# Kernel optimization log

Measured on AMD Instinct MI355X. Metric: run time of the kernel, lower is better.

## Reference

```python
import jax, jax.numpy as jnp
import numpy as np

S, HID = 2048, 4096
H, KV, D = 32, 8, 128
EPS = 1e-6
THETA = 10000.0


def setup_inputs() -> dict:
    key = jax.random.key(0)
    k0, k1, k2 = jax.random.split(key, 3)
    return {
        "positions": jnp.arange(S, dtype=jnp.int32),
        "hidden_states": jax.random.normal(k0, (S, HID), jnp.float32),
        "w_qkv": jax.random.normal(k1, ((H + 2 * KV) * D, HID), jnp.float32) * 0.02,
        "w_o": jax.random.normal(k2, (HID, H * D), jnp.float32) * 0.02,
        "gq": jnp.ones((D,), jnp.float32),
        "gk": jnp.ones((D,), jnp.float32),
    }


def _rmsnorm(x, g):
    # per-head RMSNorm over last dim (head_dim)
    return x * jax.lax.rsqrt(jnp.mean(x * x, axis=-1, keepdims=True) + EPS) * g


def _rope(x, positions):
    # NeoX-style rotary embedding, rotary_dim == head_dim
    half = D // 2
    inv_freq = 1.0 / (THETA ** (jnp.arange(half, dtype=jnp.float32) * 2.0 / D))
    freqs = positions.astype(jnp.float32)[:, None] * inv_freq  # [S, half]
    cos = jnp.cos(freqs)[:, None, :]  # [S, 1, half]
    sin = jnp.sin(freqs)[:, None, :]
    x1, x2 = x[..., :half], x[..., half:]
    return jnp.concatenate([x1 * cos - x2 * sin, x2 * cos + x1 * sin], axis=-1)


def reference(positions, hidden_states, w_qkv, w_o, gq, gk):
    qkv = hidden_states @ w_qkv.T  # [S, (H+2KV)*D]
    q = qkv[:, : H * D].reshape(S, H, D)
    k = qkv[:, H * D : (H + KV) * D].reshape(S, KV, D)
    v = qkv[:, (H + KV) * D :].reshape(S, KV, D)

    q = _rmsnorm(q, gq)
    k = _rmsnorm(k, gk)
    q = _rope(q, positions)
    k = _rope(k, positions)

    rep = H // KV
    kf = jnp.repeat(k, rep, axis=1)  # [S, H, D]
    vf = jnp.repeat(v, rep, axis=1)

    scale = D ** -0.5
    scores = jnp.einsum("qhd,khd->hqk", q, kf) * scale  # [H, S, S]
    causal = jnp.tril(jnp.ones((S, S), dtype=bool))
    scores = jnp.where(causal[None], scores, jnp.finfo(scores.dtype).min)
    attn = jax.nn.softmax(scores, axis=-1)
    ctx = jnp.einsum("hqk,khd->qhd", attn, vf).reshape(S, H * D)
    return ctx @ w_o.T  # [S, HID]
```

## Files before the change

kernel.cpp:

```cpp
#include <hip/hip_runtime.h>
#include <hip/hip_bf16.h>

#define S_LEN 2048
#define HID   4096
#define NH    32
#define NKV   8
#define DH    128
#define NQKV  ((NH + 2*NKV) * DH)

typedef __attribute__((ext_vector_type(8))) short s16x8;
typedef __attribute__((ext_vector_type(4))) short s16x4;
typedef __attribute__((ext_vector_type(4))) float f32x4;

__device__ __forceinline__ short f2bf(float x) {
    union { __hip_bfloat16 b; short s; } u;
    u.b = __float2bfloat16(x);
    return u.s;
}
__device__ __forceinline__ float bf2f(short s) {
    union { unsigned int u; float f; } v;
    v.u = ((unsigned int)(unsigned short)s) << 16;
    return v.f;
}

__device__ __forceinline__ void gload16(const void* g, void* l) {
    __builtin_amdgcn_global_load_lds(
        (const __attribute__((address_space(1))) void*)g,
        (__attribute__((address_space(3))) void*)l,
        16, 0, 0);
}

__device__ __forceinline__ void cstore(float* p, float v) { *p = v; }
__device__ __forceinline__ void cstore(short* p, float v) { *p = f2bf(v); }

__global__ __launch_bounds__(256) void convert_hs_wqkv(
        const float* __restrict__ in1, short* __restrict__ o1, long n1,
        const float* __restrict__ in2, short* __restrict__ o2, long n2)
{
    const long total = n1 + n2;
    long i0 = ((long)blockIdx.x * blockDim.x + threadIdx.x) * 4;
    long stride = (long)gridDim.x * blockDim.x * 4;
    for (long i = i0; i < total; i += stride) {
        const float* src; short* dst; long off;
        if (i < n1) { src = in1; dst = o1; off = i; }
        else        { src = in2; dst = o2; off = i - n1; }
        float4 v = *(const float4*)(src + off);
        s16x4 o;
        o[0] = f2bf(v.x); o[1] = f2bf(v.y); o[2] = f2bf(v.z); o[3] = f2bf(v.w);
        *(s16x4*)(dst + off) = o;
    }
}

template <typename OT>
__global__ __launch_bounds__(256, 2) void gemm192(
        const short* __restrict__ A, const short* __restrict__ B,
        OT* __restrict__ C, int M, int N, int K)
{
    __shared__ char lds[81920];
    const int t = threadIdx.x;
    const int w = t >> 6, l = t & 63, g = l >> 4, q16 = l & 15;
    const int wm = w >> 1, wn = w & 1;
    const int bx = blockIdx.x, by = blockIdx.y;
    const int NT = K >> 6;

    const int srow = t >> 3;
    const int schunk = (t & 7) ^ (srow & 7);
    unsigned goffA[4], goffB[6];
#pragma unroll
    for (int i = 0; i < 4; ++i)
        goffA[i] = (unsigned)(((by * 128 + i * 32 + srow) * K) * 2 + schunk * 16);
#pragma unroll
    for (int i = 0; i < 6; ++i)
        goffB[i] = (unsigned)(((bx * 192 + i * 32 + srow) * K) * 2 + schunk * 16);
    const int dstw = w * 1024;

    auto STAGE = [&](int kt) {
        const int par = kt & 1;
        char* dA = lds + par * 16384 + dstw;
        char* dB = lds + 32768 + par * 24576 + dstw;
        const unsigned kb = (unsigned)kt * 128;
#pragma unroll
        for (int i = 0; i < 4; ++i)
            gload16((const char*)A + (goffA[i] + kb), dA + i * 4096);
#pragma unroll
        for (int i = 0; i < 6; ++i)
            gload16((const char*)B + (goffB[i] + kb), dB + i * 4096);
    };

    int aoff[4], boff[6];
#pragma unroll
    for (int mi = 0; mi < 4; ++mi) aoff[mi] = (wm * 64 + mi * 16 + q16) * 128;
#pragma unroll
    for (int ni = 0; ni < 6; ++ni) boff[ni] = (wn * 96 + ni * 16 + q16) * 128;
    const int sw0 = ((g) ^ (q16 & 7)) << 4;
    const int sw1 = ((4 + g) ^ (q16 & 7)) << 4;

    f32x4 acc[4][6] = {};
    s16x8 aE[4][2], aO[4][2], b0f[3][2], b1f[3][2];

    STAGE(0); STAGE(1);
    asm volatile("s_waitcnt vmcnt(10)" ::: "memory");
    __builtin_amdgcn_s_barrier();
    {
        const char* A0 = lds;
#pragma unroll
        for (int mi = 0; mi < 4; ++mi) {
            aE[mi][0] = *(const s16x8*)(A0 + aoff[mi] + sw0);
            aE[mi][1] = *(const s16x8*)(A0 + aoff[mi] + sw1);
        }
    }

#define GB(KT, AC, AN, PAR) do {                                              \
    const char* Bs_ = lds + 32768 + (PAR) * 24576;                            \
    _Pragma("unroll")                                                         \
    for (int ni = 0; ni < 3; ++ni) {                                          \
        b0f[ni][0] = *(const s16x8*)(Bs_ + boff[ni] + sw0);                   \
        b0f[ni][1] = *(const s16x8*)(Bs_ + boff[ni] + sw1);                   \
    }                                                                         \
    _Pragma("unroll")                                                         \
    for (int ni = 0; ni < 3; ++ni) {                                          \
        b1f[ni][0] = *(const s16x8*)(Bs_ + boff[3 + ni] + sw0);               \
        b1f[ni][1] = *(const s16x8*)(Bs_ + boff[3 + ni] + sw1);               \
    }                                                                         \
    asm volatile("s_waitcnt lgkmcnt(6)" ::: "memory");       \
    __builtin_amdgcn_sched_barrier(0);                                        \
    __builtin_amdgcn_s_setprio(1);                                            \
    _Pragma("unroll")                                                         \
    for (int mi = 0; mi < 4; ++mi)                                            \
    _Pragma("unroll")                                                         \
    for (int ni = 0; ni < 3; ++ni)                                            \
    _Pragma("unroll")                                                         \
    for (int kk = 0; kk < 2; ++kk)                                            \
        acc[mi][ni] = __builtin_amdgcn_mfma_f32_16x16x32_bf16(                \
                AC[mi][kk], b0f[ni][kk], acc[mi][ni], 0, 0, 0);               \
    __builtin_amdgcn_s_setprio(0);                                            \
    asm volatile("s_waitcnt lgkmcnt(0)" ::: "memory");           \
    __builtin_amdgcn_sched_barrier(0);                                        \
    asm volatile("s_waitcnt vmcnt(0)" ::: "memory");        \
    __builtin_amdgcn_s_barrier();       \
    if ((KT) + 2 < NT) STAGE((KT) + 2);                                       \
    if ((KT) + 1 < NT) {                      \
        const char* An_ = lds + (((PAR) ^ 1) * 16384);                        \
        _Pragma("unroll")                                                     \
        for (int mi = 0; mi < 4; ++mi) {                                      \
            AN[mi][0] = *(const s16x8*)(An_ + aoff[mi] + sw0);                \
            AN[mi][1] = *(const s16x8*)(An_ + aoff[mi] + sw1);                \
        }                                                                     \
    }                                                                         \
    __builtin_amdgcn_s_setprio(1);                                            \
    _Pragma("unroll")                                                         \
    for (int mi = 0; mi < 4; ++mi)                                            \
    _Pragma("unroll")                                                         \
    for (int ni = 0; ni < 3; ++ni)                                            \
    _Pragma("unroll")                                                         \
    for (int kk = 0; kk < 2; ++kk)                                            \
        acc[mi][3 + ni] = __builtin_amdgcn_mfma_f32_16x16x32_bf16(            \
                AC[mi][kk], b1f[ni][kk], acc[mi][3 + ni], 0, 0, 0);           \
    __builtin_amdgcn_s_setprio(0);                                            \
} while (0)

    for (int kt = 0; kt < NT; kt += 2) {
        GB(kt,     aE, aO, 0);
        GB(kt + 1, aO, aE, 1);
    }
#undef GB

#pragma unroll
    for (int mi = 0; mi < 4; ++mi) {
        long row = (long)by * 128 + wm * 64 + mi * 16 + g * 4;
#pragma unroll
        for (int ni = 0; ni < 6; ++ni) {
            long col = (long)bx * 192 + wn * 96 + ni * 16 + q16;
            f32x4 v = acc[mi][ni];
#pragma unroll
            for (int r = 0; r < 4; ++r)
                cstore(&C[(row + r) * (long)N + col], v[r]);
        }
    }
}

template <typename OT>
__global__ __launch_bounds__(256, 2) void gemm_bt(
        const short* __restrict__ A, const short* __restrict__ B,
        OT* __restrict__ C, int M, int N, int K)
{
    __shared__ char lds[65536];
    const int t = threadIdx.x;
    const int w = t >> 6, l = t & 63, g = l >> 4, q16 = l & 15;
    const int wm = w >> 1, wn = w & 1;
    const int bx = blockIdx.x, by = blockIdx.y;
    const int NT = K >> 6;

    const int srow = t >> 3;
    const int schunk = (t & 7) ^ (srow & 7);
    unsigned goffA[4], goffB[4];
#pragma unroll
    for (int i = 0; i < 4; ++i) {
        goffA[i] = (unsigned)(((by * 128 + i * 32 + srow) * K) * 2 + schunk * 16);
        goffB[i] = (unsigned)(((bx * 128 + i * 32 + srow) * K) * 2 + schunk * 16);
    }
    const int dstw = w * 1024;

    auto STAGE = [&](int kt) {
        const int par = kt & 1;
        char* dA = lds + par * 16384 + dstw;
        char* dB = lds + 32768 + par * 16384 + dstw;
        const unsigned kb = (unsigned)kt * 128;
#pragma unroll
        for (int i = 0; i < 4; ++i) {
            gload16((const char*)A + (goffA[i] + kb), dA + i * 4096);
            gload16((const char*)B + (goffB[i] + kb), dB + i * 4096);
        }
    };

    int aoff[4], boff[4];
#pragma unroll
    for (int i = 0; i < 4; ++i) {
        aoff[i] = (wm * 64 + i * 16 + q16) * 128;
        boff[i] = (wn * 64 + i * 16 + q16) * 128;
    }
    const int sw0 = ((g) ^ (q16 & 7)) << 4;
    const int sw1 = ((4 + g) ^ (q16 & 7)) << 4;

    f32x4 acc[4][4] = {};
    s16x8 aE[4][2], aO[4][2], bf[4][2];

    STAGE(0); STAGE(1);
    asm volatile("s_waitcnt vmcnt(8)" ::: "memory");
    __builtin_amdgcn_s_barrier();
    {
        const char* A0 = lds;
#pragma unroll
        for (int mi = 0; mi < 4; ++mi) {
            aE[mi][0] = *(const s16x8*)(A0 + aoff[mi] + sw0);
            aE[mi][1] = *(const s16x8*)(A0 + aoff[mi] + sw1);
        }
    }

#define GB(KT, AC, AN, PAR) do {                                              \
    const char* Bs_ = lds + 32768 + (PAR) * 16384;                            \
    _Pragma("unroll")                                                         \
    for (int ni = 0; ni < 4; ++ni) {                                          \
        bf[ni][0] = *(const s16x8*)(Bs_ + boff[ni] + sw0);                    \
        bf[ni][1] = *(const s16x8*)(Bs_ + boff[ni] + sw1);                    \
    }                                                                         \
    asm volatile("s_waitcnt lgkmcnt(4)" ::: "memory");      \
    __builtin_amdgcn_sched_barrier(0);                                        \
    __builtin_amdgcn_s_setprio(1);                                            \
    _Pragma("unroll")                                                         \
    for (int mi = 0; mi < 4; ++mi)                                            \
    _Pragma("unroll")                                                         \
    for (int ni = 0; ni < 2; ++ni)                                            \
    _Pragma("unroll")                                                         \
    for (int kk = 0; kk < 2; ++kk)                                            \
        acc[mi][ni] = __builtin_amdgcn_mfma_f32_16x16x32_bf16(                \
                AC[mi][kk], bf[ni][kk], acc[mi][ni], 0, 0, 0);                \
    __builtin_amdgcn_s_setprio(0);                                            \
    asm volatile("s_waitcnt lgkmcnt(0)" ::: "memory");          \
    __builtin_amdgcn_sched_barrier(0);                                        \
    asm volatile("s_waitcnt vmcnt(0)" ::: "memory");        \
    __builtin_amdgcn_s_barrier();       \
    if ((KT) + 2 < NT) STAGE((KT) + 2);                                       \
    if ((KT) + 1 < NT) {                      \
        const char* An_ = lds + (((PAR) ^ 1) * 16384);                        \
        _Pragma("unroll")                                                     \
        for (int mi = 0; mi < 4; ++mi) {                                      \
            AN[mi][0] = *(const s16x8*)(An_ + aoff[mi] + sw0);                \
            AN[mi][1] = *(const s16x8*)(An_ + aoff[mi] + sw1);                \
        }                                                                     \
    }                                                                         \
    __builtin_amdgcn_s_setprio(1);                                            \
    _Pragma("unroll")                                                         \
    for (int mi = 0; mi < 4; ++mi)                                            \
    _Pragma("unroll")                                                         \
    for (int ni = 0; ni < 2; ++ni)                                            \
    _Pragma("unroll")                                                         \
    for (int kk = 0; kk < 2; ++kk)                                            \
        acc[mi][2 + ni] = __builtin_amdgcn_mfma_f32_16x16x32_bf16(            \
                AC[mi][kk], bf[2 + ni][kk], acc[mi][2 + ni], 0, 0, 0);        \
    __builtin_amdgcn_s_setprio(0);                                            \
} while (0)

    for (int kt = 0; kt < NT; kt += 2) {
        GB(kt,     aE, aO, 0);
        GB(kt + 1, aO, aE, 1);
    }
#undef GB

#pragma unroll
    for (int mi = 0; mi < 4; ++mi) {
        long row = (long)by * 128 + wm * 64 + mi * 16 + g * 4;
#pragma unroll
        for (int ni = 0; ni < 4; ++ni) {
            long col = (long)bx * 128 + wn * 64 + ni * 16 + q16;
            f32x4 v = acc[mi][ni];
#pragma unroll
            for (int r = 0; r < 4; ++r)
                cstore(&C[(row + r) * (long)N + col], v[r]);
        }
    }
}

__global__ __launch_bounds__(256) void post_gemm1_fused(
        const float* __restrict__ wo, short* __restrict__ wob,
        const short* __restrict__ qkvb, const int* __restrict__ pos,
        const float* __restrict__ gq, const float* __restrict__ gk,
        short* __restrict__ qo, short* __restrict__ ko,
        short* __restrict__ vt)
{
    const int bid = blockIdx.x;

    if (bid < 2048) {
        const long n = (long)HID * (NH * DH);
        long i0 = ((long)bid * 256 + threadIdx.x) * 4;
        long stride = 2048L * 256 * 4;
        for (long i = i0; i < n; i += stride) {
            float4 v = *(const float4*)(wo + i);
            s16x4 o;
            o[0] = f2bf(v.x); o[1] = f2bf(v.y); o[2] = f2bf(v.z); o[3] = f2bf(v.w);
            *(s16x4*)(wob + i) = o;
        }
        return;
    }

    if (bid < 12288) {
        const int idx = bid - 2048;
        const int s = idx / 5;
        const int slot = (idx % 5) * 8 + (threadIdx.x >> 5);
        const int p = threadIdx.x & 31, d = p * 4;

        s16x4 xv = *(const s16x4*)(qkvb + (long)s * NQKV + slot * DH + d);
        float x[4];
#pragma unroll
        for (int r = 0; r < 4; ++r) x[r] = bf2f(xv[r]);

        float ss = x[0]*x[0] + x[1]*x[1] + x[2]*x[2] + x[3]*x[3];
#pragma unroll
        for (int o = 1; o < 32; o <<= 1) ss += __shfl_xor(ss, o);
        float rms = rsqrtf(ss * (1.0f / DH) + 1e-6f);

        const bool isq = slot < NH;
        const float* gp = isq ? gq : gk;
        float y[4];
#pragma unroll
        for (int r = 0; r < 4; ++r) y[r] = x[r] * rms * gp[d + r];

        float y2[4];
#pragma unroll
        for (int r = 0; r < 4; ++r) y2[r] = __shfl_xor(y[r], 16);

        const float po = (float)pos[s];
        const int jbase = d & 63;
        s16x4 ov;
#pragma unroll
        for (int r = 0; r < 4; ++r) {
            float invf = exp2f(-(float)(jbase + r) * (13.287712379549449f / 64.0f));
            float ang = po * invf;
            float c = cosf(ang), sn = sinf(ang);
            float outv = (d < 64) ? (y[r] * c - y2[r] * sn)
                                  : (y[r] * c + y2[r] * sn);
            ov[r] = f2bf(outv);
        }
        if (isq) *(s16x4*)(qo + ((long)s * NH + slot) * DH + d) = ov;
        else     *(s16x4*)(ko + ((long)s * NKV + (slot - NH)) * DH + d) = ov;
        return;
    }

    __shared__ short tile[64][72];
    const int idx2 = bid - 12288;
    const int sb = idx2 & 31, db = (idx2 >> 5) & 1, h = idx2 >> 6;
    const int t = threadIdx.x;
#pragma unroll
    for (int i = 0; i < 2; ++i) {
        int c = i * 256 + t;
        int row = c >> 3, dc = (c & 7) * 8;
        const short* src = qkvb + (long)(sb*64 + row) * NQKV
                           + (NH + NKV + h) * DH + db*64 + dc;
        s16x8 x = *(const s16x8*)src;
#pragma unroll
        for (int jj = 0; jj < 8; ++jj) tile[row][dc + jj] = x[jj];
    }
    __syncthreads();
#pragma unroll
    for (int i = 0; i < 2; ++i) {
        int c = i * 256 + t;
        int dr = c >> 3, sc = (c & 7) * 8;
        s16x8 y;
#pragma unroll
        for (int jj = 0; jj < 8; ++jj) y[jj] = tile[sc + jj][dr];
        short* dst = vt + (long)(h*DH + db*64 + dr) * S_LEN + sb*64 + sc;
        *(s16x8*)dst = y;
    }
}

__device__ __forceinline__ void stage_kv(const char* kgB, const char* vgB,
                                         int kt, int t, char* kd, char* vd)
{
    const int w = t >> 6;
#pragma unroll
    for (int ci = 0; ci < 4; ++ci) {
        int c = ci * 256 + t;
        int row = c >> 4, col16 = c & 15;
        const char* gk = kgB + (long)(kt*64 + row) * (NKV*DH*2)
                         + ((col16*16) ^ ((row & 7) << 4));
        gload16(gk, kd + ci*4096 + w*1024);
        int rowv = c >> 3, scol8 = c & 7;
        const char* gv = vgB + (long)rowv * (S_LEN*2) + kt*128
                         + ((scol8*16) ^ ((rowv & 7) << 4));
        gload16(gv, vd + ci*4096 + w*1024);
    }
}

__global__ __launch_bounds__(256, 2) void attn_kernel(
        const short* __restrict__ qg, const short* __restrict__ kg,
        const short* __restrict__ vtg, short* __restrict__ ctx)
{
    const int bx = blockIdx.x;
    const int h  = bx & 31;
    const int slot = bx >> 5;
    const int qb = (slot < 8) ? slot : 23 - slot;
    const int kvh = h >> 2;
    const int t = threadIdx.x, w = t >> 6, l = t & 63, g = l >> 4, q16 = l & 15;

    __shared__ char Kl[2][16384];
    __shared__ char Vl[2][16384];
    __shared__ short Pl[4][32 * 64];

    const float scale = 0.08838834764831845f;
    const char* kgB = (const char*)kg + (long)kvh * DH * 2;
    const char* vgB = (const char*)vtg + (long)kvh * DH * (long)S_LEN * 2;

    const int nt = 2 * qb + 2;
    int qrow[2];
    qrow[0] = qb*128 + w*32 + q16;
    qrow[1] = qrow[0] + 16;

    s16x8 qf[2][4];
#pragma unroll
    for (int s = 0; s < 2; ++s) {
        const short* qptr = qg + ((long)qrow[s] * NH + h) * DH;
#pragma unroll
        for (int dk = 0; dk < 4; ++dk)
            qf[s][dk] = *(const s16x8*)(qptr + dk*32 + g*8);
    }

    f32x4 oacc[2][8] = {};
    float m_run[2] = {-1e30f, -1e30f}, l_run[2] = {0.f, 0.f};

    stage_kv(kgB, vgB, 0, t, Kl[0], Vl[0]);
    __syncthreads();

    for (int kt = 0; kt < nt; ++kt) {
        const int b = kt & 1;
        if (kt + 1 < nt)
            stage_kv(kgB, vgB, kt + 1, t, Kl[b ^ 1], Vl[b ^ 1]);
        const char* kb = Kl[b];
        const char* vbb = Vl[b];

        f32x4 sacc[2][4] = {};
        __builtin_amdgcn_s_setprio(1);
#pragma unroll
        for (int m = 0; m < 4; ++m) {
            int kvr = m*16 + q16;
            s16x8 af[4];
#pragma unroll
            for (int dk = 0; dk < 4; ++dk) {
                int byte = (kvr*256 + (dk*32 + g*8)*2) ^ ((kvr & 7) << 4);
                af[dk] = *(const s16x8*)(kb + byte);
            }
#pragma unroll
            for (int s = 0; s < 2; ++s)
#pragma unroll
                for (int dk = 0; dk < 4; ++dk)
                    sacc[s][m] = __builtin_amdgcn_mfma_f32_16x16x32_bf16(
                            af[dk], qf[s][dk], sacc[s][m], 0,0,0);
        }
        __builtin_amdgcn_s_setprio(0);

        const bool diag = (kt >= 2*qb);
        float mx[2];
#pragma unroll
        for (int s = 0; s < 2; ++s) {
            mx[s] = -1e30f;
#pragma unroll
            for (int m = 0; m < 4; ++m)
#pragma unroll
                for (int r = 0; r < 4; ++r) {
                    float x = sacc[s][m][r] * scale;
                    if (diag) {
                        int kv = kt*64 + m*16 + g*4 + r;
                        if (kv > qrow[s]) x = -1e30f;
                    }
                    sacc[s][m][r] = x;
                    mx[s] = fmaxf(mx[s], x);
                }
            mx[s] = fmaxf(mx[s], __shfl_xor(mx[s], 16));
            mx[s] = fmaxf(mx[s], __shfl_xor(mx[s], 32));
        }
        if (__any((mx[0] > m_run[0] + 8.f) || (mx[1] > m_run[1] + 8.f))) {
#pragma unroll
            for (int s = 0; s < 2; ++s) {
                float m_new = fmaxf(m_run[s], mx[s]);
                float corr = __expf(m_run[s] - m_new);
                l_run[s] *= corr;
                m_run[s] = m_new;
                float rf[4];
#pragma unroll
                for (int r = 0; r < 4; ++r)
                    rf[r] = __shfl(corr, (g << 4) | (g*4 + r));
#pragma unroll
                for (int nf = 0; nf < 8; ++nf)
#pragma unroll
                    for (int r = 0; r < 4; ++r) oacc[s][nf][r] *= rf[r];
            }
        }
#pragma unroll
        for (int s = 0; s < 2; ++s) {
            float psum = 0.f;
#pragma unroll
            for (int m = 0; m < 4; ++m) {
                s16x4 pk;
#pragma unroll
                for (int r = 0; r < 4; ++r) {
                    float e = __expf(sacc[s][m][r] - m_run[s]);
                    psum += e;
                    pk[r] = f2bf(e);
                }
                int byte = ((s*16 + q16)*128 + (m*16 + g*4)*2) ^ ((q16 & 7) << 4);
                *(s16x4*)((char*)&Pl[w][0] + byte) = pk;
            }
            psum += __shfl_xor(psum, 16);
            psum += __shfl_xor(psum, 32);
            l_run[s] += psum;
        }

        __builtin_amdgcn_s_setprio(1);
#pragma unroll
        for (int ks = 0; ks < 2; ++ks) {
            s16x8 pa[2];
#pragma unroll
            for (int s = 0; s < 2; ++s) {
                int pbyte = ((s*16 + q16)*128 + (ks*32 + g*8)*2) ^ ((q16 & 7) << 4);
                pa[s] = *(const s16x8*)((const char*)&Pl[w][0] + pbyte);
            }
#pragma unroll
            for (int nf = 0; nf < 8; ++nf) {
                int drow = nf*16 + q16;
                int vbyte = (drow*128 + (ks*32 + g*8)*2) ^ ((drow & 7) << 4);
                s16x8 vbf = *(const s16x8*)(vbb + vbyte);
#pragma unroll
                for (int s = 0; s < 2; ++s)
                    oacc[s][nf] = __builtin_amdgcn_mfma_f32_16x16x32_bf16(
                            pa[s], vbf, oacc[s][nf], 0,0,0);
            }
        }
        __builtin_amdgcn_s_setprio(0);
        __syncthreads();
    }

#pragma unroll
    for (int s = 0; s < 2; ++s) {
        float lr[4];
#pragma unroll
        for (int r = 0; r < 4; ++r)
            lr[r] = __shfl(l_run[s], (g << 4) | (g*4 + r));
#pragma unroll
        for (int nf = 0; nf < 8; ++nf)
#pragma unroll
            for (int r = 0; r < 4; ++r) {
                int row = qb*128 + w*32 + s*16 + g*4 + r;
                int col = h*DH + nf*16 + q16;
                float val = oacc[s][nf][r] / lr[r];
                ctx[(long)row * (NH*DH) + col] = f2bf(val);
            }
    }
}

extern "C" void kernel_launch(void* const* d_in, const int* in_sizes, int n_in,
                              void* d_out, int out_size, void* d_ws, size_t ws_size,
                              hipStream_t stream)
{
    const int*   positions = (const int*)  d_in[0];
    const float* hs        = (const float*)d_in[1];
    const float* wqkv      = (const float*)d_in[2];
    const float* wo        = (const float*)d_in[3];
    const float* gq        = (const float*)d_in[4];
    const float* gk        = (const float*)d_in[5];
    float* out = (float*)d_out;
    char* ws = (char*)d_ws;

    const size_t MB = 1ull << 20;
    short* hsb   = (short*)(ws);
    short* ctxb  = (short*)(ws);
    short* wqkvb = (short*)(ws + 16*MB);
    short* wob   = (short*)(ws + 16*MB);
    short* vtbuf = (short*)(ws + 48*MB);
    short* qkvb  = (short*)(ws + 67*MB);
    short* qbuf  = (short*)(ws + 91*MB);
    short* kbuf  = (short*)(ws + 107*MB);

    (void)in_sizes; (void)n_in; (void)out_size; (void)ws_size;

    convert_hs_wqkv<<<2048, 256, 0, stream>>>(
            hs, hsb, (long)S_LEN * HID,
            wqkv, wqkvb, (long)NQKV * HID);
    gemm192<short><<<dim3(NQKV/192, S_LEN/128), 256, 0, stream>>>(
            hsb, wqkvb, qkvb, S_LEN, NQKV, HID);
    post_gemm1_fused<<<12800, 256, 0, stream>>>(
            wo, wob, qkvb, positions, gq, gk, qbuf, kbuf, vtbuf);
    attn_kernel<<<dim3(512), 256, 0, stream>>>(qbuf, kbuf, vtbuf, ctxb);
    gemm_bt<float><<<dim3(HID/128, S_LEN/128), 256, 0, stream>>>(
            ctxb, wob, out, S_LEN, HID, HID);
}
```

Baseline: 299.9 us.

## Enlarge QKV GEMM tile to 256x192 with 8 waves and phased LDS pipeline

The QKV projection GEMM moves from a 128x192 tile with 4 waves to a 256x192 tile with 8 waves (512 threads). Each wave now owns 128x48 of the output. A unified double-buffered LDS layout of 112 KB replaces the old separate A/B buffers. The main loop is split into four phases per k-tile, each with barriers between LDS reads and MFMA bursts. The goal is more operand reuse per tile and fewer global loads per flop, at the cost of many more workgroup barriers, a much larger LDS footprint that likely limits occupancy to one block per CU, and fewer blocks in the grid.

```diff
diff --git a/kernel.cpp b/kernel.cpp
--- a/kernel.cpp
+++ b/kernel.cpp
@@ -52,125 +52,108 @@
 }
 
 template <typename OT>
-__global__ __launch_bounds__(256, 2) void gemm192(
+__global__ __launch_bounds__(512, 2) void gemm192(
         const short* __restrict__ A, const short* __restrict__ B,
         OT* __restrict__ C, int M, int N, int K)
 {
-    __shared__ char lds[81920];
+    __shared__ char lds[114688];
     const int t = threadIdx.x;
     const int w = t >> 6, l = t & 63, g = l >> 4, q16 = l & 15;
-    const int wm = w >> 1, wn = w & 1;
+    const int wm = w >> 2, wn = w & 3;
     const int bx = blockIdx.x, by = blockIdx.y;
     const int NT = K >> 6;
 
     const int srow = t >> 3;
     const int schunk = (t & 7) ^ (srow & 7);
-    unsigned goffA[4], goffB[6];
+    unsigned gA[4], gB[3];
 #pragma unroll
     for (int i = 0; i < 4; ++i)
-        goffA[i] = (unsigned)(((by * 128 + i * 32 + srow) * K) * 2 + schunk * 16);
-#pragma unroll
-    for (int i = 0; i < 6; ++i)
-        goffB[i] = (unsigned)(((bx * 192 + i * 32 + srow) * K) * 2 + schunk * 16);
+        gA[i] = (unsigned)(((by * 256 + i * 64 + srow) * K) * 2 + schunk * 16);
+#pragma unroll
+    for (int i = 0; i < 3; ++i)
+        gB[i] = (unsigned)(((bx * 192 + i * 64 + srow) * K) * 2 + schunk * 16);
     const int dstw = w * 1024;
 
     auto STAGE = [&](int kt) {
-        const int par = kt & 1;
-        char* dA = lds + par * 16384 + dstw;
-        char* dB = lds + 32768 + par * 24576 + dstw;
+        char* d = lds + (kt & 1) * 57344 + dstw;
         const unsigned kb = (unsigned)kt * 128;
 #pragma unroll
         for (int i = 0; i < 4; ++i)
-            gload16((const char*)A + (goffA[i] + kb), dA + i * 4096);
-#pragma unroll
-        for (int i = 0; i < 6; ++i)
-            gload16((const char*)B + (goffB[i] + kb), dB + i * 4096);
+            gload16((const char*)A + (gA[i] + kb), d + i * 8192);
+#pragma unroll
+        for (int i = 0; i < 3; ++i)
+            gload16((const char*)B + (gB[i] + kb), d + 32768 + i * 8192);
     };
 
-    int aoff[4], boff[6];
-#pragma unroll
-    for (int mi = 0; mi < 4; ++mi) aoff[mi] = (wm * 64 + mi * 16 + q16) * 128;
-#pragma unroll
-    for (int ni = 0; ni < 6; ++ni) boff[ni] = (wn * 96 + ni * 16 + q16) * 128;
+    int aoff[8], boff[3];
+#pragma unroll
+    for (int mi = 0; mi < 8; ++mi) aoff[mi] = (wm * 128 + mi * 16 + q16) * 128;
+#pragma unroll
+    for (int ni = 0; ni < 3; ++ni) boff[ni] = (wn * 48 + ni * 16 + q16) * 128;
     const int sw0 = ((g) ^ (q16 & 7)) << 4;
     const int sw1 = ((4 + g) ^ (q16 & 7)) << 4;
 
-    f32x4 acc[4][6] = {};
-    s16x8 aE[4][2], aO[4][2], b0f[3][2], b1f[3][2];
+    f32x4 acc[8][3] = {};
+    s16x8 a[4], b[3];
 
     STAGE(0); STAGE(1);
-    asm volatile("s_waitcnt vmcnt(10)" ::: "memory");
+    asm volatile("s_waitcnt vmcnt(7)" ::: "memory");
+    __builtin_amdgcn_sched_barrier(0);
     __builtin_amdgcn_s_barrier();
-    {
-        const char* A0 = lds;
-#pragma unroll
-        for (int mi = 0; mi < 4; ++mi) {
-            aE[mi][0] = *(const s16x8*)(A0 + aoff[mi] + sw0);
-            aE[mi][1] = *(const s16x8*)(A0 + aoff[mi] + sw1);
-        }
-    }
-
-#define GB(KT, AC, AN, PAR) do {                                              \
-    const char* Bs_ = lds + 32768 + (PAR) * 24576;                            \
-    _Pragma("unroll")                                                         \
-    for (int ni = 0; ni < 3; ++ni) {                                          \
-        b0f[ni][0] = *(const s16x8*)(Bs_ + boff[ni] + sw0);                   \
-        b0f[ni][1] = *(const s16x8*)(Bs_ + boff[ni] + sw1);                   \
+
+#define PH(PAR, SUB, RB, SW) do {                                             \
+    const char* Ab_ = lds + (PAR) * 57344;                                    \
+    _Pragma("unroll")                                                         \
+    for (int j = 0; j < 4; ++j)                                               \
+        a[j] = *(const s16x8*)(Ab_ + aoff[(SUB) * 4 + j] + (SW));             \
+    if (RB) {                                                                 \
+        const char* Bb_ = Ab_ + 32768;                                        \
+        _Pragma("unroll")                                                     \
+        for (int ni = 0; ni < 3; ++ni)                                        \
+            b[ni] = *(const s16x8*)(Bb_ + boff[ni] + (SW));                   \
     }                                                                         \
-    _Pragma("unroll")                                                         \
-    for (int ni = 0; ni < 3; ++ni) {                                          \
-        b1f[ni][0] = *(const s16x8*)(Bs_ + boff[3 + ni] + sw0);               \
-        b1f[ni][1] = *(const s16x8*)(Bs_ + boff[3 + ni] + sw1);               \
-    }                                                                         \
-    asm volatile("s_waitcnt lgkmcnt(6)" ::: "memory");       \
+    __builtin_amdgcn_s_barrier();                                             \
+    asm volatile("s_waitcnt lgkmcnt(0)" ::: "memory");                        \
     __builtin_amdgcn_sched_barrier(0);                                        \
     __builtin_amdgcn_s_setprio(1);                                            \
     _Pragma("unroll")                                                         \
-    for (int mi = 0; mi < 4; ++mi)                                            \
+    for (int j = 0; j < 4; ++j)                                               \
     _Pragma("unroll")                                                         \
     for (int ni = 0; ni < 3; ++ni)                                            \
-    _Pragma("unroll")                                                         \
-    for (int kk = 0; kk < 2; ++kk)                                            \
-        acc[mi][ni] = __builtin_amdgcn_mfma_f32_16x16x32_bf16(                \
-                AC[mi][kk], b0f[ni][kk], acc[mi][ni], 0, 0, 0);               \
+        acc[(SUB) * 4 + j][ni] = __builtin_amdgcn_mfma_f32_16x16x32_bf16(     \
+                a[j], b[ni], acc[(SUB) * 4 + j][ni], 0, 0, 0);                \
     __builtin_amdgcn_s_setprio(0);                                            \
-    asm volatile("s_waitcnt lgkmcnt(0)" ::: "memory");           \
+    __builtin_amdgcn_s_barrier();                                             \
+} while (0)
+
+#define TILE(KT, PAR) do {                                                    \
+    PH(PAR, 0, 1, sw0);                         \
+    PH(PAR, 1, 0, sw0);                         \
+    PH(PAR, 0, 1, sw1);                         \
+    PH(PAR, 1, 0, sw1);                         \
+    if ((KT) + 2 < NT) {                                                      \
+        STAGE((KT) + 2);       \
+        asm volatile("s_waitcnt vmcnt(7)" ::: "memory");      \
+    } else {                                                                  \
+        asm volatile("s_waitcnt vmcnt(0)" ::: "memory");                      \
+    }                                                                         \
     __builtin_amdgcn_sched_barrier(0);                                        \
-    asm volatile("s_waitcnt vmcnt(0)" ::: "memory");        \
-    __builtin_amdgcn_s_barrier();       \
-    if ((KT) + 2 < NT) STAGE((KT) + 2);                                       \
-    if ((KT) + 1 < NT) {                      \
-        const char* An_ = lds + (((PAR) ^ 1) * 16384);                        \
-        _Pragma("unroll")                                                     \
-        for (int mi = 0; mi < 4; ++mi) {                                      \
-            AN[mi][0] = *(const s16x8*)(An_ + aoff[mi] + sw0);                \
-            AN[mi][1] = *(const s16x8*)(An_ + aoff[mi] + sw1);                \
-        }                                                                     \
-    }                                                                         \
-    __builtin_amdgcn_s_setprio(1);                                            \
-    _Pragma("unroll")                                                         \
-    for (int mi = 0; mi < 4; ++mi)                                            \
-    _Pragma("unroll")                                                         \
-    for (int ni = 0; ni < 3; ++ni)                                            \
-    _Pragma("unroll")                                                         \
-    for (int kk = 0; kk < 2; ++kk)                                            \
-        acc[mi][3 + ni] = __builtin_amdgcn_mfma_f32_16x16x32_bf16(            \
-                AC[mi][kk], b1f[ni][kk], acc[mi][3 + ni], 0, 0, 0);           \
-    __builtin_amdgcn_s_setprio(0);                                            \
+    __builtin_amdgcn_s_barrier();               \
 } while (0)
 
     for (int kt = 0; kt < NT; kt += 2) {
-        GB(kt,     aE, aO, 0);
-        GB(kt + 1, aO, aE, 1);
-    }
-#undef GB
-
-#pragma unroll
-    for (int mi = 0; mi < 4; ++mi) {
-        long row = (long)by * 128 + wm * 64 + mi * 16 + g * 4;
-#pragma unroll
-        for (int ni = 0; ni < 6; ++ni) {
-            long col = (long)bx * 192 + wn * 96 + ni * 16 + q16;
+        TILE(kt,     0);
+        TILE(kt + 1, 1);
+    }
+#undef TILE
+#undef PH
+
+#pragma unroll
+    for (int mi = 0; mi < 8; ++mi) {
+        long row = (long)by * 256 + wm * 128 + mi * 16 + g * 4;
+#pragma unroll
+        for (int ni = 0; ni < 3; ++ni) {
+            long col = (long)bx * 192 + wn * 48 + ni * 16 + q16;
             f32x4 v = acc[mi][ni];
 #pragma unroll
             for (int r = 0; r < 4; ++r)
@@ -604,7 +587,7 @@
     convert_hs_wqkv<<<2048, 256, 0, stream>>>(
             hs, hsb, (long)S_LEN * HID,
             wqkv, wqkvb, (long)NQKV * HID);
-    gemm192<short><<<dim3(NQKV/192, S_LEN/128), 256, 0, stream>>>(
+    gemm192<short><<<dim3(NQKV/192, S_LEN/256), 512, 0, stream>>>(
             hsb, wqkvb, qkvb, S_LEN, NQKV, HID);
     post_gemm1_fused<<<12800, 256, 0, stream>>>(
             wo, wob, qkvb, positions, gq, gk, qbuf, kbuf, vtbuf);
```

After: 304.2 us. Within noise of the previous version (+1.4%).
